# Optimization experiments

Hardware: AMD Instinct MI355X
Metric: run time of the kernel (lower is better)

The kernel has to match this reference:

```python
import jax, jax.numpy as jnp
import numpy as np

N = 100000
E = 1200000
NFEAT = 64
NCLASS = 64


def setup_inputs() -> dict:
    key = jax.random.key(0)
    k1, k2, k3, k4, k5, k6 = jax.random.split(key, 6)
    x = jax.random.normal(k1, (N, NFEAT), dtype=jnp.float32)
    edge_row = jax.random.randint(k2, (E,), 0, N, dtype=jnp.int32).astype(jnp.int64)
    edge_col = jax.random.randint(k3, (E,), 0, N, dtype=jnp.int32).astype(jnp.int64)
    edge_weight = jax.random.uniform(k4, (E,), dtype=jnp.float32)
    W = jax.random.normal(k5, (NCLASS, NFEAT), dtype=jnp.float32) / np.sqrt(NFEAT)
    b = jax.random.normal(k6, (NCLASS,), dtype=jnp.float32) * 0.01
    return {"x": x, "edge_row": edge_row, "edge_col": edge_col,
            "edge_weight": edge_weight, "W": W, "b": b, "k": 2}


def _spmm(edge_row, edge_col, edge_weight, x):
    # out[i] = sum_{e: row[e]==i} w[e] * x[col[e]]  == (sparse adj) @ x
    msgs = edge_weight[:, None] * x[edge_col]          # [E, F]
    return jax.ops.segment_sum(msgs, edge_row, num_segments=N)


def reference(x, edge_row, edge_col, edge_weight, W, b, k):
    h = x
    for _ in range(k):  # k is a small static int (propagation depth)
        h = _spmm(edge_row, edge_col, edge_weight, h)
    return h @ W.T + b  # nn.Linear(nfeat, nclass)
```

## Files before the change

kernel.cpp:

```cpp
#include <hip/hip_runtime.h>
#include <hip/hip_fp16.h>

#define FF 64
#define RPB 128
#define RCAP 2048
#define PAIRCAP 2432
#define PCHUNK 4096
#define NBCNT 782

typedef _Float16 f16x8 __attribute__((ext_vector_type(8)));
typedef float    f32x4 __attribute__((ext_vector_type(4)));


union HU { unsigned int u; __half2 h; };

__device__ __forceinline__ unsigned int f2h2(float a, float b) {
    HU t; t.h = __floats2half2_rn(a, b);
    return t.u;
}
__device__ __forceinline__ __half2 u2h2(unsigned int u) {
    HU t; t.u = u;
    return t.h;
}


__global__ void cvt_and_count(const float* __restrict__ x, unsigned short* __restrict__ xh,
                              int nelem, const int* __restrict__ erow,
                              int* __restrict__ cnts, int E, int partBlocks) {
    __shared__ int lcnt[NBCNT];
    int t = threadIdx.x;

    if ((int)blockIdx.x >= partBlocks) {
        int i = ((blockIdx.x - partBlocks) * 256 + t) * 4;
        if (i < nelem) {
            float4 v = *(const float4*)&x[i];
            uint2 st;
            st.x = f2h2(v.x, v.y);
            st.y = f2h2(v.z, v.w);
            *(uint2*)&xh[i] = st;
        }
        return;
    }

    for (int i = t; i < NBCNT; i += 256) lcnt[i] = 0;
    __syncthreads();
    int base = blockIdx.x * PCHUNK;
    int lim  = min(PCHUNK, E - base);
    for (int i = t; i < lim; i += 256)
        atomicAdd(&lcnt[erow[base + i] >> 7], 1);
    __syncthreads();
    for (int i = t; i < NBCNT; i += 256)
        cnts[(size_t)i * partBlocks + blockIdx.x] = lcnt[i];
}


__global__ void scan_bases(const int* __restrict__ cnts, int* __restrict__ bases,
                           int* __restrict__ bcount, int nb) {
    __shared__ int s[256];
    int bkt = blockIdx.x, t = threadIdx.x;
    const int* c = cnts + (size_t)bkt * nb;
    int* bs = bases + (size_t)bkt * nb;

    int v0 = (t < nb) ? c[t] : 0;
    s[t] = v0; __syncthreads();
    for (int off = 1; off < 256; off <<= 1) {
        int a = (t >= off) ? s[t - off] : 0;
        __syncthreads();
        s[t] += a;
        __syncthreads();
    }
    int ex0 = s[t] - v0;
    int tot0 = s[255];
    __syncthreads();

    int v1 = (t + 256 < nb) ? c[t + 256] : 0;
    s[t] = v1; __syncthreads();
    for (int off = 1; off < 256; off <<= 1) {
        int a = (t >= off) ? s[t - off] : 0;
        __syncthreads();
        s[t] += a;
        __syncthreads();
    }
    int ex1 = tot0 + s[t] - v1;
    int tot = tot0 + s[255];

    if (t < nb)       bs[t]       = bkt * RCAP + ex0;
    if (t + 256 < nb) bs[t + 256] = bkt * RCAP + ex1;
    if (t == 0)       bcount[bkt] = tot;
}


__global__ void scatter(const int* __restrict__ erow, const int* __restrict__ ecol,
                        const float* __restrict__ ew, const int* __restrict__ bases,
                        uint2* __restrict__ bent, int E, int partBlocks) {
    __shared__ int bas[NBCNT];
    __shared__ int cur[NBCNT];
    int b = blockIdx.x, t = threadIdx.x;
    for (int i = t; i < NBCNT; i += 256) {
        bas[i] = bases[(size_t)i * partBlocks + b];
        cur[i] = 0;
    }
    __syncthreads();

    int base = b * PCHUNK;
    int lim  = min(PCHUNK, E - base);
    for (int i = t; i < lim; i += 256) {
        int e = base + i;
        int r = erow[e];
        int bkt = r >> 7;
        int off = atomicAdd(&cur[bkt], 1);
        uint2 en;
        en.x = ((unsigned)(r & (RPB - 1)) << 17) | (unsigned)ecol[e];
        en.y = (unsigned)__float_as_int(ew[e]);
        bent[bas[bkt] + off] = en;
    }
}


__device__ __forceinline__ void build_lds_csr_g(const uint2* __restrict__ src, int cnt,
                                                int2* pairLds, int* deg, int* pofs,
                                                int* cur, int* part, int t, int nthr) {
    if (t < RPB) { deg[t] = 0; cur[t] = 0; }
    __syncthreads();
    for (int i = t; i < cnt; i += nthr)
        atomicAdd(&deg[src[i].x >> 17], 1);
    __syncthreads();

    if (t < RPB) part[t] = (deg[t] + 3) & ~3;
    __syncthreads();
    for (int off = 1; off < RPB; off <<= 1) {
        int add = (t < RPB && t >= off) ? part[t - off] : 0;
        __syncthreads();
        if (t < RPB) part[t] += add;
        __syncthreads();
    }
    if (t < RPB) pofs[t] = part[t] - ((deg[t] + 3) & ~3);
    __syncthreads();

    for (int i = t; i < cnt; i += nthr) {
        uint2 e = src[i];
        int lr  = e.x >> 17;
        int col = e.x & 0x1FFFF;
        float w = __int_as_float((int)e.y);
        int pos = pofs[lr] + atomicAdd(&cur[lr], 1);
        pairLds[pos] = make_int2(col, (int)f2h2(w, w));
    }
    if (t < RPB) {
        int a = deg[t], p = (a + 3) & ~3;
        for (int q = a; q < p; ++q) pairLds[pofs[t] + q] = make_int2(0, 0);
    }
    __syncthreads();
}


__device__ __forceinline__ void pkfma4(__half2 w2, uint4 v, __half2 acc[4]) {
    acc[0] = __hfma2(w2, u2h2(v.x), acc[0]);
    acc[1] = __hfma2(w2, u2h2(v.y), acc[1]);
    acc[2] = __hfma2(w2, u2h2(v.z), acc[2]);
    acc[3] = __hfma2(w2, u2h2(v.w), acc[3]);
}

__device__ __forceinline__ void row_accum8_lds(const int4* __restrict__ p, int n4,
                                               const uint4* __restrict__ hin4,
                                               int lg, __half2 acc[4]) {
    if (n4 <= 0) return;
    int4 q0 = p[0];
    int4 q1 = p[1];
    uint4 v0 = hin4[(size_t)q0.x * 8 + lg];
    uint4 v1 = hin4[(size_t)q0.z * 8 + lg];
    uint4 v2 = hin4[(size_t)q1.x * 8 + lg];
    uint4 v3 = hin4[(size_t)q1.z * 8 + lg];
    for (int i = 2; i < n4; i += 2) {
        int4 r0 = p[i];
        int4 r1 = p[i + 1];
        uint4 u0 = hin4[(size_t)r0.x * 8 + lg];
        uint4 u1 = hin4[(size_t)r0.z * 8 + lg];
        uint4 u2 = hin4[(size_t)r1.x * 8 + lg];
        uint4 u3 = hin4[(size_t)r1.z * 8 + lg];
        pkfma4(u2h2((unsigned)q0.y), v0, acc);
        pkfma4(u2h2((unsigned)q0.w), v1, acc);
        pkfma4(u2h2((unsigned)q1.y), v2, acc);
        pkfma4(u2h2((unsigned)q1.w), v3, acc);
        q0 = r0; q1 = r1;
        v0 = u0; v1 = u1; v2 = u2; v3 = u3;
    }
    pkfma4(u2h2((unsigned)q0.y), v0, acc);
    pkfma4(u2h2((unsigned)q0.w), v1, acc);
    pkfma4(u2h2((unsigned)q1.y), v2, acc);
    pkfma4(u2h2((unsigned)q1.w), v3, acc);
}


__global__ __launch_bounds__(512) void spmm1(const uint2* __restrict__ bent,
        const int* __restrict__ bcount, const unsigned short* __restrict__ hin,
        unsigned short* __restrict__ hout, int Nn) {
    __shared__ int2 pairLds[PAIRCAP];
    __shared__ int  deg[RPB], pofs[RPB], cur[RPB], part[RPB];
    const uint4* hin4 = (const uint4*)hin;
    int b = blockIdx.x, t = threadIdx.x;
    int cnt = min(bcount[b], RCAP);

    build_lds_csr_g(bent + (size_t)b * RCAP, cnt, pairLds, deg, pofs, cur, part, t, 512);

    int lane = t & 63, g = lane >> 3, lg = lane & 7;
    int rbase = (t >> 6) * 8 + g;
#pragma unroll
    for (int pass = 0; pass < 2; ++pass) {
        int rloc = pass * 64 + rbase;
        int row  = b * RPB + rloc;
        __half2 acc[4] = {__half2{0,0}, __half2{0,0}, __half2{0,0}, __half2{0,0}};
        int plen = (deg[rloc] + 3) & ~3;
        row_accum8_lds((const int4*)pairLds + (pofs[rloc] >> 1), plen >> 1, hin4, lg, acc);
        if (row < Nn)
            ((uint4*)hout)[(size_t)row * 8 + lg] = *(const uint4*)acc;
    }
}


__global__ __launch_bounds__(512) void spmm2(const uint2* __restrict__ bent,
        const int* __restrict__ bcount, const unsigned short* __restrict__ hin,
        const float* __restrict__ Wm, const float* __restrict__ bias,
        float* __restrict__ out, int Nn) {
    __shared__ int2 pairLds[PAIRCAP];
    __shared__ int  deg[RPB], pofs[RPB], cur[RPB], part[RPB];
    __shared__ unsigned short shw[64][72];
    __shared__ unsigned short shh[128][72];
    __shared__ float sbias[64];
    const uint4* hin4 = (const uint4*)hin;
    int b = blockIdx.x, t = threadIdx.x;
    int cnt = min(bcount[b], RCAP);

    for (int i = t; i < 1024; i += 512) {
        int idx = i * 4;
        int c = idx >> 6, f = idx & 63;
        float4 w4 = *(const float4*)&Wm[idx];
        uint2 pk;
        pk.x = f2h2(w4.x, w4.y);
        pk.y = f2h2(w4.z, w4.w);
        *(uint2*)&shw[c][f] = pk;
    }
    if (t < 64) sbias[t] = bias[t];

    build_lds_csr_g(bent + (size_t)b * RCAP, cnt, pairLds, deg, pofs, cur, part, t, 512);

    int lane = t & 63, g = lane >> 3, lg = lane & 7;
    int rbase = (t >> 6) * 8 + g;
#pragma unroll
    for (int pass = 0; pass < 2; ++pass) {
        int rloc = pass * 64 + rbase;
        __half2 acc[4] = {__half2{0,0}, __half2{0,0}, __half2{0,0}, __half2{0,0}};
        int plen = (deg[rloc] + 3) & ~3;
        row_accum8_lds((const int4*)pairLds + (pofs[rloc] >> 1), plen >> 1, hin4, lg, acc);
        *(uint4*)&shh[rloc][lg * 8] = *(const uint4*)acc;
    }
    __syncthreads();

    int tt = t >> 6;
    int mr = lane & 15, kg = lane >> 4;
    f32x4 c0 = {0.f,0.f,0.f,0.f}, c1 = {0.f,0.f,0.f,0.f};
    f32x4 c2 = {0.f,0.f,0.f,0.f}, c3 = {0.f,0.f,0.f,0.f};
#pragma unroll
    for (int kc = 0; kc < 2; ++kc) {
        int k0 = kc * 32 + kg * 8;
        f16x8 a  = *(const f16x8*)&shh[tt * 16 + mr][k0];
        f16x8 b0 = *(const f16x8*)&shw[mr][k0];
        f16x8 b1 = *(const f16x8*)&shw[16 + mr][k0];
        f16x8 b2 = *(const f16x8*)&shw[32 + mr][k0];
        f16x8 b3 = *(const f16x8*)&shw[48 + mr][k0];
        c0 = __builtin_amdgcn_mfma_f32_16x16x32_f16(a, b0, c0, 0, 0, 0);
        c1 = __builtin_amdgcn_mfma_f32_16x16x32_f16(a, b1, c1, 0, 0, 0);
        c2 = __builtin_amdgcn_mfma_f32_16x16x32_f16(a, b2, c2, 0, 0, 0);
        c3 = __builtin_amdgcn_mfma_f32_16x16x32_f16(a, b3, c3, 0, 0, 0);
    }
#pragma unroll
    for (int j = 0; j < 4; ++j) {
        int orow = b * RPB + tt * 16 + kg * 4 + j;
        if (orow < Nn) {
            float* op = &out[(size_t)orow * FF];
            op[mr]      = c0[j] + sbias[mr];
            op[16 + mr] = c1[j] + sbias[16 + mr];
            op[32 + mr] = c2[j] + sbias[32 + mr];
            op[48 + mr] = c3[j] + sbias[48 + mr];
        }
    }
}


extern "C" void kernel_launch(void* const* d_in, const int* in_sizes, int n_in,
                              void* d_out, int out_size, void* d_ws, size_t ws_size,
                              hipStream_t stream) {
    const float* x    = (const float*)d_in[0];
    const int*   erow = (const int*)  d_in[1];
    const int*   ecol = (const int*)  d_in[2];
    const float* ew   = (const float*)d_in[3];
    const float* W    = (const float*)d_in[4];
    const float* b    = (const float*)d_in[5];

    int E  = in_sizes[1];
    int Nn = in_sizes[0] / FF;
    int nelem = Nn * FF;
    int NB = (Nn + RPB - 1) / RPB;
    int partBlocks = (E + PCHUNK - 1) / PCHUNK;
    int cvtBlocks  = (nelem / 4 + 255) / 256;

    char*  ws  = (char*)d_ws;
    size_t off = 0;
    auto alloc = [&](size_t bytes) { void* p = ws + off; off += (bytes + 255) & ~255ULL; return p; };
    unsigned short* xh   = (unsigned short*)alloc((size_t)nelem * 2);
    unsigned short* h1h  = (unsigned short*)alloc((size_t)nelem * 2);
    uint2*          bent = (uint2*)alloc((size_t)NB * RCAP * sizeof(uint2));
    int* cnts   = (int*)alloc((size_t)NBCNT * partBlocks * sizeof(int));
    int* bases  = (int*)alloc((size_t)NBCNT * partBlocks * sizeof(int));
    int* bcount = (int*)alloc(NBCNT * sizeof(int));

    cvt_and_count<<<partBlocks + cvtBlocks, 256, 0, stream>>>(
        x, xh, nelem, erow, cnts, E, partBlocks);
    scan_bases<<<NBCNT, 256, 0, stream>>>(cnts, bases, bcount, partBlocks);
    scatter<<<partBlocks, 256, 0, stream>>>(erow, ecol, ew, bases, bent, E, partBlocks);

    spmm1<<<NB, 512, 0, stream>>>(bent, bcount, xh, h1h, Nn);
    spmm2<<<NB, 512, 0, stream>>>(bent, bcount, h1h, W, b, (float*)d_out, Nn);
}
```

Baseline: 96.16 us.

## Persist per-block LDS CSR from spmm1 to global and reuse it in spmm2

Result: no change. 97.15 us (+1.0%).

```diff
diff --git a/kernel.cpp b/kernel.cpp
--- a/kernel.cpp
+++ b/kernel.cpp
@@ -114,42 +114,6 @@
         en.y = (unsigned)__float_as_int(ew[e]);
         bent[bas[bkt] + off] = en;
     }
-}
-
-
-__device__ __forceinline__ void build_lds_csr_g(const uint2* __restrict__ src, int cnt,
-                                                int2* pairLds, int* deg, int* pofs,
-                                                int* cur, int* part, int t, int nthr) {
-    if (t < RPB) { deg[t] = 0; cur[t] = 0; }
-    __syncthreads();
-    for (int i = t; i < cnt; i += nthr)
-        atomicAdd(&deg[src[i].x >> 17], 1);
-    __syncthreads();
-
-    if (t < RPB) part[t] = (deg[t] + 3) & ~3;
-    __syncthreads();
-    for (int off = 1; off < RPB; off <<= 1) {
-        int add = (t < RPB && t >= off) ? part[t - off] : 0;
-        __syncthreads();
-        if (t < RPB) part[t] += add;
-        __syncthreads();
-    }
-    if (t < RPB) pofs[t] = part[t] - ((deg[t] + 3) & ~3);
-    __syncthreads();
-
-    for (int i = t; i < cnt; i += nthr) {
-        uint2 e = src[i];
-        int lr  = e.x >> 17;
-        int col = e.x & 0x1FFFF;
-        float w = __int_as_float((int)e.y);
-        int pos = pofs[lr] + atomicAdd(&cur[lr], 1);
-        pairLds[pos] = make_int2(col, (int)f2h2(w, w));
-    }
-    if (t < RPB) {
-        int a = deg[t], p = (a + 3) & ~3;
-        for (int q = a; q < p; ++q) pairLds[pofs[t] + q] = make_int2(0, 0);
-    }
-    __syncthreads();
 }
 
 
@@ -193,14 +157,61 @@
 
 __global__ __launch_bounds__(512) void spmm1(const uint2* __restrict__ bent,
         const int* __restrict__ bcount, const unsigned short* __restrict__ hin,
-        unsigned short* __restrict__ hout, int Nn) {
+        unsigned short* __restrict__ hout, int2* __restrict__ rs2G,
+        int2* __restrict__ pairG, int* __restrict__ ptot, int Nn) {
     __shared__ int2 pairLds[PAIRCAP];
     __shared__ int  deg[RPB], pofs[RPB], cur[RPB], part[RPB];
     const uint4* hin4 = (const uint4*)hin;
     int b = blockIdx.x, t = threadIdx.x;
     int cnt = min(bcount[b], RCAP);
-
-    build_lds_csr_g(bent + (size_t)b * RCAP, cnt, pairLds, deg, pofs, cur, part, t, 512);
+    const uint2* src = bent + (size_t)b * RCAP;
+
+    uint2 ereg[4];
+#pragma unroll
+    for (int k = 0; k < 4; ++k) {
+        int i = t + k * 512;
+        if (i < cnt) ereg[k] = src[i];
+    }
+    if (t < RPB) { deg[t] = 0; cur[t] = 0; }
+    __syncthreads();
+#pragma unroll
+    for (int k = 0; k < 4; ++k)
+        if (t + k * 512 < cnt) atomicAdd(&deg[ereg[k].x >> 17], 1);
+    __syncthreads();
+
+    if (t < RPB) part[t] = (deg[t] + 3) & ~3;
+    __syncthreads();
+    for (int off = 1; off < RPB; off <<= 1) {
+        int add = (t < RPB && t >= off) ? part[t - off] : 0;
+        __syncthreads();
+        if (t < RPB) part[t] += add;
+        __syncthreads();
+    }
+    if (t < RPB) pofs[t] = part[t] - ((deg[t] + 3) & ~3);
+    __syncthreads();
+
+#pragma unroll
+    for (int k = 0; k < 4; ++k)
+        if (t + k * 512 < cnt) {
+            uint2 e = ereg[k];
+            int lr  = e.x >> 17;
+            int col = e.x & 0x1FFFF;
+            float w = __int_as_float((int)e.y);
+            int pos = pofs[lr] + atomicAdd(&cur[lr], 1);
+            pairLds[pos] = make_int2(col, (int)f2h2(w, w));
+        }
+    if (t < RPB) {
+        int a = deg[t], p = (a + 3) & ~3;
+        for (int q = a; q < p; ++q) pairLds[pofs[t] + q] = make_int2(0, 0);
+    }
+    __syncthreads();
+
+    int totPad = pofs[RPB - 1] + ((deg[RPB - 1] + 3) & ~3);
+    int4* pg = (int4*)(pairG + (size_t)b * PAIRCAP);
+    for (int i = t; i < (totPad >> 1); i += 512)
+        pg[i] = ((const int4*)pairLds)[i];
+    if (t < RPB) rs2G[(size_t)b * RPB + t] = make_int2(pofs[t], (deg[t] + 3) & ~3);
+    if (t == 0) ptot[b] = totPad;
 
     int lane = t & 63, g = lane >> 3, lg = lane & 7;
     int rbase = (t >> 6) * 8 + g;
@@ -217,19 +228,27 @@
 }
 
 
-__global__ __launch_bounds__(512) void spmm2(const uint2* __restrict__ bent,
-        const int* __restrict__ bcount, const unsigned short* __restrict__ hin,
+__global__ __launch_bounds__(512) void spmm2(const int2* __restrict__ rs2G,
+        const int2* __restrict__ pairG, const int* __restrict__ ptot,
+        const unsigned short* __restrict__ hin,
         const float* __restrict__ Wm, const float* __restrict__ bias,
         float* __restrict__ out, int Nn) {
     __shared__ int2 pairLds[PAIRCAP];
-    __shared__ int  deg[RPB], pofs[RPB], cur[RPB], part[RPB];
+    __shared__ int  pofs[RPB], plen[RPB];
     __shared__ unsigned short shw[64][72];
     __shared__ unsigned short shh[128][72];
     __shared__ float sbias[64];
     const uint4* hin4 = (const uint4*)hin;
     int b = blockIdx.x, t = threadIdx.x;
-    int cnt = min(bcount[b], RCAP);
-
+
+    int totPad = ptot[b];
+    const int4* pg = (const int4*)(pairG + (size_t)b * PAIRCAP);
+    for (int i = t; i < (totPad >> 1); i += 512)
+        ((int4*)pairLds)[i] = pg[i];
+    if (t < RPB) {
+        int2 r = rs2G[(size_t)b * RPB + t];
+        pofs[t] = r.x; plen[t] = r.y;
+    }
     for (int i = t; i < 1024; i += 512) {
         int idx = i * 4;
         int c = idx >> 6, f = idx & 63;
@@ -240,8 +259,7 @@
         *(uint2*)&shw[c][f] = pk;
     }
     if (t < 64) sbias[t] = bias[t];
-
-    build_lds_csr_g(bent + (size_t)b * RCAP, cnt, pairLds, deg, pofs, cur, part, t, 512);
+    __syncthreads();
 
     int lane = t & 63, g = lane >> 3, lg = lane & 7;
     int rbase = (t >> 6) * 8 + g;
@@ -249,8 +267,8 @@
     for (int pass = 0; pass < 2; ++pass) {
         int rloc = pass * 64 + rbase;
         __half2 acc[4] = {__half2{0,0}, __half2{0,0}, __half2{0,0}, __half2{0,0}};
-        int plen = (deg[rloc] + 3) & ~3;
-        row_accum8_lds((const int4*)pairLds + (pofs[rloc] >> 1), plen >> 1, hin4, lg, acc);
+        row_accum8_lds((const int4*)pairLds + (pofs[rloc] >> 1), plen[rloc] >> 1,
+                       hin4, lg, acc);
         *(uint4*)&shh[rloc][lg * 8] = *(const uint4*)acc;
     }
     __syncthreads();
@@ -309,15 +327,18 @@
     unsigned short* xh   = (unsigned short*)alloc((size_t)nelem * 2);
     unsigned short* h1h  = (unsigned short*)alloc((size_t)nelem * 2);
     uint2*          bent = (uint2*)alloc((size_t)NB * RCAP * sizeof(uint2));
+    int2*           pairG = (int2*)alloc((size_t)NB * PAIRCAP * sizeof(int2));
+    int2*           rs2G  = (int2*)alloc((size_t)NB * RPB * sizeof(int2));
     int* cnts   = (int*)alloc((size_t)NBCNT * partBlocks * sizeof(int));
     int* bases  = (int*)alloc((size_t)NBCNT * partBlocks * sizeof(int));
     int* bcount = (int*)alloc(NBCNT * sizeof(int));
+    int* ptot   = (int*)alloc(NBCNT * sizeof(int));
 
     cvt_and_count<<<partBlocks + cvtBlocks, 256, 0, stream>>>(
         x, xh, nelem, erow, cnts, E, partBlocks);
     scan_bases<<<NBCNT, 256, 0, stream>>>(cnts, bases, bcount, partBlocks);
     scatter<<<partBlocks, 256, 0, stream>>>(erow, ecol, ew, bases, bent, E, partBlocks);
 
-    spmm1<<<NB, 512, 0, stream>>>(bent, bcount, xh, h1h, Nn);
-    spmm2<<<NB, 512, 0, stream>>>(bent, bcount, h1h, W, b, (float*)d_out, Nn);
-}
+    spmm1<<<NB, 512, 0, stream>>>(bent, bcount, xh, h1h, rs2G, pairG, ptot, Nn);
+    spmm2<<<NB, 512, 0, stream>>>(rs2G, pairG, ptot, h1h, W, b, (float*)d_out, Nn);
+}
```
